# Kernel optimization log

Hardware: AMD Instinct MI355X
Metric: run time of the kernel (lower is better)

## Reference

```python
import jax, jax.numpy as jnp
import numpy as np

N = 50000   # nodes
E = 800000  # edges
G = 64      # graphs in the batch
DIN = 128
DOUT = 256


def _lin(key, fan_in, fan_out):
    s = 1.0 / np.sqrt(fan_in)
    kw, kb = jax.random.split(key)
    W = jax.random.uniform(kw, (fan_in, fan_out), jnp.float32, -s, s)
    b = jax.random.uniform(kb, (fan_out,), jnp.float32, -s, s)
    return W, b


def setup_inputs() -> dict:
    key = jax.random.key(0)
    ks = jax.random.split(key, 12)
    x = jax.random.normal(ks[0], (N, DIN), jnp.float32)
    edge_index = jax.random.randint(ks[1], (2, E), 0, N, dtype=jnp.int64)
    batch = jnp.sort(jax.random.randint(ks[2], (N,), 0, G, dtype=jnp.int64))
    W1, b1 = _lin(ks[3], DIN, 128)
    W2, b2 = _lin(ks[4], 128, 128)
    W3, b3 = _lin(ks[5], 128, 128)
    A1, ba1 = _lin(ks[6], DIN, 64)
    A2, ba2 = _lin(ks[7], 64, 32)
    A3, ba3 = _lin(ks[8], 32, 1)
    M1, bm1 = _lin(ks[9], 128, 128)
    M2, bm2 = _lin(ks[10], 128, DOUT)
    return dict(x=x, edge_index=edge_index, batch=batch,
                W1=W1, b1=b1, W2=W2, b2=b2, W3=W3, b3=b3,
                A1=A1, ba1=ba1, A2=A2, ba2=ba2, A3=A3, ba3=ba3,
                M1=M1, bm1=bm1, M2=M2, bm2=bm2)


def _gcn_norm(edge_index, n, dtype):
    # GCNConv default: add self-loops, symmetric normalization D^-1/2 (A+I) D^-1/2
    loop = jnp.arange(n, dtype=edge_index.dtype)
    src = jnp.concatenate([edge_index[0], loop])
    dst = jnp.concatenate([edge_index[1], loop])
    deg = jax.ops.segment_sum(jnp.ones_like(dst, dtype), dst, num_segments=n)
    dinv = jnp.where(deg > 0, jax.lax.rsqrt(deg), 0.0)
    return src, dst, dinv[src] * dinv[dst]


def _gcn(h, W, b, src, dst, norm, n):
    h = h @ W                                   # [N, F_out]
    msg = h[src] * norm[:, None]                # gather + scale (memory bound)
    return jax.ops.segment_sum(msg, dst, num_segments=n) + b


def _segment_softmax(w, batch, g):
    # per-graph softmax (PyG softmax): stabilize with segment max
    m = jax.ops.segment_max(w, batch, num_segments=g)
    e = jnp.exp(w - m[batch])
    s = jax.ops.segment_sum(e, batch, num_segments=g)
    return e / (s[batch] + 1e-16)


def reference(x, edge_index, batch,
              W1, b1, W2, b2, W3, b3,
              A1, ba1, A2, ba2, A3, ba3,
              M1, bm1, M2, bm2):
    n = x.shape[0]
    src, dst, norm = _gcn_norm(edge_index, n, x.dtype)
    relu = jax.nn.relu
    # feature branch
    f = relu(_gcn(x, W1, b1, src, dst, norm, n))
    f = relu(_gcn(f, W2, b2, src, dst, norm, n))
    f = relu(_gcn(f, W3, b3, src, dst, norm, n))
    # attention branch
    w = relu(_gcn(x, A1, ba1, src, dst, norm, n))
    w = relu(_gcn(w, A2, ba2, src, dst, norm, n))
    w = relu(_gcn(w, A3, ba3, src, dst, norm, n))   # [N, 1]
    w = _segment_softmax(w, batch, G)
    # attention-weighted sum pooling per graph
    pooled = jax.ops.segment_sum(f * w, batch, num_segments=G)  # [G, 128]
    # MLP([128,128,256], batch_norm=False): Linear+ReLU, plain last Linear
    out = relu(pooled @ M1 + bm1) @ M2 + bm2
    return out
```

## Files before the change

### kernel.cpp

```cpp
#include <hip/hip_runtime.h>
#include <hip/hip_fp16.h>
#include <math.h>


#define DIN 128
#define FH  128
#define DOUT 256
#define NBUK 128
#define SUBN 512
#define IMGCAP 16384
#define ECAP 16384

typedef float f4 __attribute__((ext_vector_type(4)));
typedef float f32x4 __attribute__((ext_vector_type(4)));
typedef _Float16 h8v __attribute__((ext_vector_type(8)));
typedef _Float16 h4v __attribute__((ext_vector_type(4)));


__global__ __launch_bounds__(256) void scan1_kernel(const int* __restrict__ cnt,
        int* __restrict__ bsum, float* __restrict__ dinv, int n) {
    __shared__ int sm[256];
    int tid = threadIdx.x;
    int base = blockIdx.x * 512;
    int a = (base + tid < n) ? cnt[base + tid] : 0;
    int b = (base + 256 + tid < n) ? cnt[base + 256 + tid] : 0;
    if (base + tid < n)       dinv[base + tid]       = rsqrtf((float)(a + 1));
    if (base + 256 + tid < n) dinv[base + 256 + tid] = rsqrtf((float)(b + 1));
    sm[tid] = a + b;
    __syncthreads();
    for (int off = 128; off > 0; off >>= 1) {
        if (tid < off) sm[tid] += sm[tid + off];
        __syncthreads();
    }
    if (tid == 0) bsum[blockIdx.x] = sm[0];
}

__global__ void scan2_kernel(const int* __restrict__ bsum, int* __restrict__ boff,
                             int* __restrict__ rpN, int nb) {
    if (threadIdx.x == 0) {
        int run = 0;
        for (int i = 0; i < nb; ++i) { boff[i] = run; run += bsum[i]; }
        *rpN = run;
    }
}

__global__ __launch_bounds__(256) void scan3_kernel(const int* __restrict__ cnt,
        const int* __restrict__ boff, int* __restrict__ rp, int n) {
    __shared__ int sm[256];
    int tid = threadIdx.x;
    int base = blockIdx.x * 512;
    int i0 = base + 2 * tid;
    int c0 = (i0 < n) ? cnt[i0] : 0;
    int c1 = (i0 + 1 < n) ? cnt[i0 + 1] : 0;
    int ps = c0 + c1;
    sm[tid] = ps;
    __syncthreads();
    for (int off = 1; off < 256; off <<= 1) {
        int v = (tid >= off) ? sm[tid - off] : 0;
        __syncthreads();
        sm[tid] += v;
        __syncthreads();
    }
    int excl = sm[tid] - ps + boff[blockIdx.x];
    if (i0 < n) rp[i0] = excl;
    if (i0 + 1 < n) rp[i0 + 1] = excl + c0;
}

__global__ __launch_bounds__(256) void ebucket_kernel(const int* __restrict__ src,
        const int* __restrict__ dst, int* __restrict__ bcur,
        unsigned long long* __restrict__ entries, int E, int shift) {
    __shared__ int lcnt[NBUK], lscan[NBUK], lbase[NBUK], lcur[NBUK];
    __shared__ unsigned long long stage[2048];
    const int tid = threadIdx.x;
    const int e0 = blockIdx.x * 2048;
    if (tid < NBUK) { lcnt[tid] = 0; lcur[tid] = 0; }
    __syncthreads();
    int s_[8], d_[8];
    #pragma unroll
    for (int k = 0; k < 8; ++k) {
        int e = e0 + k * 256 + tid;
        if (e < E) {
            s_[k] = src[e];
            d_[k] = dst[e];
            atomicAdd(&lcnt[d_[k] >> shift], 1);
        } else {
            d_[k] = -1;
        }
    }
    __syncthreads();
    if (tid < NBUK) lscan[tid] = lcnt[tid];
    __syncthreads();
    for (int off = 1; off < NBUK; off <<= 1) {
        int v = 0;
        if (tid < NBUK && tid >= off) v = lscan[tid - off];
        __syncthreads();
        if (tid < NBUK) lscan[tid] += v;
        __syncthreads();
    }
    if (tid < NBUK) {
        lscan[tid] -= lcnt[tid];
        lbase[tid] = lcnt[tid] ? atomicAdd(&bcur[tid], lcnt[tid]) : 0;
    }
    __syncthreads();
    #pragma unroll
    for (int k = 0; k < 8; ++k) {
        if (d_[k] >= 0) {
            int b = d_[k] >> shift;
            int pos = lscan[b] + atomicAdd(&lcur[b], 1);
            stage[pos] = ((unsigned long long)(unsigned)d_[k] << 32) | (unsigned)s_[k];
        }
    }
    __syncthreads();
    const int total = min(2048, E - e0);
    for (int i = tid; i < total; i += 256) {
        int lo = 0, hi = NBUK - 1;
        while (lo < hi) {
            int mid = (lo + hi + 1) >> 1;
            if (lscan[mid] <= i) lo = mid; else hi = mid - 1;
        }
        int idx = lbase[lo] + (i - lscan[lo]);
        if (idx < (lo + 1) * ECAP)
            entries[(size_t)idx] = stage[i];
    }
}

__global__ __launch_bounds__(512) void ecount_kernel(
        const unsigned long long* __restrict__ entries,
        const int* __restrict__ bcur, int* __restrict__ cnt, int n, int shift) {
    __shared__ int hist[SUBN];
    const int b = blockIdx.x;
    const int n0 = b << shift;
    if (n0 >= n) return;
    const int n1 = min(n0 + SUBN, n);
    const int tid = threadIdx.x;
    hist[tid] = 0;
    __syncthreads();
    const size_t ebase = (size_t)b * ECAP;
    const int len = min(bcur[b] - b * ECAP, ECAP);
    for (int i = tid; i < len; i += 512)
        atomicAdd(&hist[(int)(entries[ebase + i] >> 32) - n0], 1);
    __syncthreads();
    if (n0 + tid < n1) cnt[n0 + tid] = hist[tid];
}

__global__ __launch_bounds__(512) void ecsr_kernel(
        const unsigned long long* __restrict__ entries,
        const int* __restrict__ rp, const float* __restrict__ dinv,
        long long* __restrict__ cn, int n, int shift) {
    __shared__ long long img[IMGCAP];
    __shared__ int hist[SUBN];
    __shared__ int lcur[SUBN];
    __shared__ int sm[SUBN];
    __shared__ float dl[SUBN];
    const int b = blockIdx.x;
    const int n0 = b << shift;
    if (n0 >= n) return;
    const int n1 = min(n0 + (1 << shift), n);
    const int base = rp[n0];
    const int len  = rp[n1] - base;
    const size_t ebase = (size_t)b * ECAP;
    const int tid = threadIdx.x;
    hist[tid] = 0;
    lcur[tid] = 0;
    if (n0 + tid < n1) dl[tid] = dinv[n0 + tid];
    __syncthreads();
    for (int i = tid; i < len; i += 512)
        atomicAdd(&hist[(int)(entries[ebase + i] >> 32) - n0], 1);
    __syncthreads();
    int v = hist[tid];
    sm[tid] = v;
    __syncthreads();
    for (int off = 1; off < SUBN; off <<= 1) {
        int t = (tid >= off) ? sm[tid - off] : 0;
        __syncthreads();
        sm[tid] += t;
        __syncthreads();
    }
    hist[tid] = sm[tid] - v;
    __syncthreads();
    const bool fits = (len <= IMGCAP);
    for (int i = tid; i < len; i += 512) {
        unsigned long long e = entries[ebase + i];
        int d  = (int)(e >> 32) - n0;
        int sx = (int)(unsigned)(e & 0xffffffffu);
        int pos = hist[d] + atomicAdd(&lcur[d], 1);
        float w = dinv[sx] * dl[d];
        long long val = (long long)(unsigned)sx | ((long long)__float_as_int(w) << 32);
        if (fits) img[pos] = val;
        else      cn[base + pos] = val;
    }
    __syncthreads();
    if (fits)
        for (int i = tid; i < len; i += 512) cn[base + i] = img[i];
}

__global__ void gstart_kernel(const int* __restrict__ batch, int* __restrict__ gstart,
                              int n, int g) {
    int t = threadIdx.x;
    if (t > g) return;
    int lo = 0, hi = n;
    while (lo < hi) {
        int mid = (lo + hi) >> 1;
        if (batch[mid] < t) lo = mid + 1; else hi = mid;
    }
    gstart[t] = lo;
}

__global__ void cvt16_kernel(const float* __restrict__ in, __half* __restrict__ outh,
                             long n8) {
    long i = (long)blockIdx.x * 256 + threadIdx.x;
    if (i >= n8) return;
    f4 a = ((const f4*)in)[2 * i];
    f4 b = ((const f4*)in)[2 * i + 1];
    __half2 h0 = __float22half2_rn(make_float2(a.x, a.y));
    __half2 h1 = __float22half2_rn(make_float2(a.z, a.w));
    __half2 h2 = __float22half2_rn(make_float2(b.x, b.y));
    __half2 h3 = __float22half2_rn(make_float2(b.z, b.w));
    uint4 st;
    st.x = *(unsigned*)&h0; st.y = *(unsigned*)&h1;
    st.z = *(unsigned*)&h2; st.w = *(unsigned*)&h3;
    ((uint4*)outh)[i] = st;
}


__device__ __forceinline__ void wsplit(const float* __restrict__ W,
        _Float16* __restrict__ Th, _Float16* __restrict__ Tl,
        int fin, int fout, int i) {
    int r = i / fout, c = i % fout;
    float w = W[i];
    _Float16 h = (_Float16)w;
    Th[c * fin + r] = h;
    Tl[c * fin + r] = (_Float16)(w - (float)h);
}

__global__ __launch_bounds__(256) void wprep_kernel(const float* __restrict__ W1,
        const float* __restrict__ W2, const float* __restrict__ W3,
        const float* __restrict__ A1, const float* __restrict__ A2,
        _Float16* __restrict__ T, int* __restrict__ bcur) {
    int i = blockIdx.x * 256 + threadIdx.x;
    if (blockIdx.x == 0 && threadIdx.x < NBUK) bcur[threadIdx.x] = threadIdx.x * ECAP;
    if (i < 16384)       wsplit(W1, T,          T + 16384,  128, 128, i);
    else if (i < 32768)  wsplit(W2, T + 32768,  T + 49152,  128, 128, i - 16384);
    else if (i < 49152)  wsplit(W3, T + 65536,  T + 81920,  128, 128, i - 32768);
    else if (i < 57344)  wsplit(A1, T + 98304,  T + 106496, 128, 64,  i - 49152);
    else if (i < 59392)  wsplit(A2, T + 114688, T + 116736, 64,  32,  i - 57344);
}


__global__ __launch_bounds__(256) void fusedl1_kernel(const float* __restrict__ Y,
        const _Float16* __restrict__ T, const float* __restrict__ b1,
        const float* __restrict__ ba1, __half* __restrict__ t2,
        __half* __restrict__ u2, int n) {
    constexpr int LSTR  = 136;
    constexpr int LSTRB = 72;
    __shared__ _Float16 Yh[64 * LSTR], Yl[64 * LSTR];
    __shared__ _Float16 Fh[64 * LSTR], Fl[64 * LSTR];
    const int tid  = threadIdx.x;
    const int w    = tid >> 6;
    const int lane = tid & 63;
    const int bk   = (lane >> 4) * 8;
    const int cl   = lane & 15;
    const long row0 = (long)blockIdx.x * 64;

    for (int i = tid; i < 64 * 32; i += 256) {
        int r = i >> 5, c4 = i & 31;
        long gr = row0 + r;
        float4 v = {0.f, 0.f, 0.f, 0.f};
        if (gr < n) v = *(const float4*)&Y[gr * 128 + c4 * 4];
        _Float16 h0 = (_Float16)v.x, h1 = (_Float16)v.y;
        _Float16 h2 = (_Float16)v.z, h3 = (_Float16)v.w;
        *(h4v*)&Yh[r * LSTR + c4 * 4] = (h4v){h0, h1, h2, h3};
        *(h4v*)&Yl[r * LSTR + c4 * 4] =
            (h4v){(_Float16)(v.x - (float)h0), (_Float16)(v.y - (float)h1),
                  (_Float16)(v.z - (float)h2), (_Float16)(v.w - (float)h3)};
    }
    __syncthreads();

    {
        const _Float16* W1h = T;
        const _Float16* W1l = T + 16384;
        h8v Bh[2][4], Bl[2][4];
        #pragma unroll
        for (int ct = 0; ct < 2; ++ct) {
            int c = w * 32 + ct * 16 + cl;
            #pragma unroll
            for (int kk = 0; kk < 4; ++kk) {
                Bh[ct][kk] = *(const h8v*)&W1h[c * 128 + kk * 32 + bk];
                Bl[ct][kk] = *(const h8v*)&W1l[c * 128 + kk * 32 + bk];
            }
        }
        f32x4 acc[4][2];
        #pragma unroll
        for (int rt = 0; rt < 4; ++rt)
            #pragma unroll
            for (int ct = 0; ct < 2; ++ct) acc[rt][ct] = (f32x4){0.f,0.f,0.f,0.f};
        #pragma unroll
        for (int rt = 0; rt < 4; ++rt) {
            int r = rt * 16 + cl;
            #pragma unroll
            for (int kk = 0; kk < 4; ++kk) {
                h8v ah = *(const h8v*)&Yh[r * LSTR + kk * 32 + bk];
                h8v al = *(const h8v*)&Yl[r * LSTR + kk * 32 + bk];
                #pragma unroll
                for (int ct = 0; ct < 2; ++ct) {
                    acc[rt][ct] = __builtin_amdgcn_mfma_f32_16x16x32_f16(ah, Bh[ct][kk], acc[rt][ct], 0, 0, 0);
                    acc[rt][ct] = __builtin_amdgcn_mfma_f32_16x16x32_f16(ah, Bl[ct][kk], acc[rt][ct], 0, 0, 0);
                    acc[rt][ct] = __builtin_amdgcn_mfma_f32_16x16x32_f16(al, Bh[ct][kk], acc[rt][ct], 0, 0, 0);
                }
            }
        }
        #pragma unroll
        for (int rt = 0; rt < 4; ++rt) {
            int rowb = rt * 16 + (lane >> 4) * 4;
            #pragma unroll
            for (int ct = 0; ct < 2; ++ct) {
                int col = w * 32 + ct * 16 + cl;
                float bv = b1[col];
                #pragma unroll
                for (int j = 0; j < 4; ++j) {
                    float v = fmaxf(acc[rt][ct][j] + bv, 0.f);
                    _Float16 h = (_Float16)v;
                    Fh[(rowb + j) * LSTR + col] = h;
                    Fl[(rowb + j) * LSTR + col] = (_Float16)(v - (float)h);
                }
            }
        }
    }
    __syncthreads();

    {
        const _Float16* W2h = T + 32768;
        const _Float16* W2l = T + 49152;
        h8v Bh[2][4], Bl[2][4];
        #pragma unroll
        for (int ct = 0; ct < 2; ++ct) {
            int c = w * 32 + ct * 16 + cl;
            #pragma unroll
            for (int kk = 0; kk < 4; ++kk) {
                Bh[ct][kk] = *(const h8v*)&W2h[c * 128 + kk * 32 + bk];
                Bl[ct][kk] = *(const h8v*)&W2l[c * 128 + kk * 32 + bk];
            }
        }
        f32x4 acc[4][2];
        #pragma unroll
        for (int rt = 0; rt < 4; ++rt)
            #pragma unroll
            for (int ct = 0; ct < 2; ++ct) acc[rt][ct] = (f32x4){0.f,0.f,0.f,0.f};
        #pragma unroll
        for (int rt = 0; rt < 4; ++rt) {
            int r = rt * 16 + cl;
            #pragma unroll
            for (int kk = 0; kk < 4; ++kk) {
                h8v ah = *(const h8v*)&Fh[r * LSTR + kk * 32 + bk];
                h8v al = *(const h8v*)&Fl[r * LSTR + kk * 32 + bk];
                #pragma unroll
                for (int ct = 0; ct < 2; ++ct) {
                    acc[rt][ct] = __builtin_amdgcn_mfma_f32_16x16x32_f16(ah, Bh[ct][kk], acc[rt][ct], 0, 0, 0);
                    acc[rt][ct] = __builtin_amdgcn_mfma_f32_16x16x32_f16(ah, Bl[ct][kk], acc[rt][ct], 0, 0, 0);
                    acc[rt][ct] = __builtin_amdgcn_mfma_f32_16x16x32_f16(al, Bh[ct][kk], acc[rt][ct], 0, 0, 0);
                }
            }
        }
        __syncthreads();
        #pragma unroll
        for (int rt = 0; rt < 4; ++rt) {
            long rbase = row0 + rt * 16 + (lane >> 4) * 4;
            #pragma unroll
            for (int ct = 0; ct < 2; ++ct) {
                int col = w * 32 + ct * 16 + cl;
                #pragma unroll
                for (int j = 0; j < 4; ++j) {
                    long r = rbase + j;
                    if (r < n) t2[r * 128 + col] = __float2half(acc[rt][ct][j]);
                }
            }
        }
    }

    {
        const _Float16* A1h = T + 98304;
        const _Float16* A1l = T + 106496;
        int c = w * 16 + cl;
        h8v Bh[4], Bl[4];
        #pragma unroll
        for (int kk = 0; kk < 4; ++kk) {
            Bh[kk] = *(const h8v*)&A1h[c * 128 + kk * 32 + bk];
            Bl[kk] = *(const h8v*)&A1l[c * 128 + kk * 32 + bk];
        }
        f32x4 acc[4];
        #pragma unroll
        for (int rt = 0; rt < 4; ++rt) acc[rt] = (f32x4){0.f,0.f,0.f,0.f};
        #pragma unroll
        for (int rt = 0; rt < 4; ++rt) {
            int r = rt * 16 + cl;
            #pragma unroll
            for (int kk = 0; kk < 4; ++kk) {
                h8v ah = *(const h8v*)&Yh[r * LSTR + kk * 32 + bk];
                h8v al = *(const h8v*)&Yl[r * LSTR + kk * 32 + bk];
                acc[rt] = __builtin_amdgcn_mfma_f32_16x16x32_f16(ah, Bh[kk], acc[rt], 0, 0, 0);
                acc[rt] = __builtin_amdgcn_mfma_f32_16x16x32_f16(ah, Bl[kk], acc[rt], 0, 0, 0);
                acc[rt] = __builtin_amdgcn_mfma_f32_16x16x32_f16(al, Bh[kk], acc[rt], 0, 0, 0);
            }
        }
        float bv = ba1[c];
        #pragma unroll
        for (int rt = 0; rt < 4; ++rt) {
            int rowb = rt * 16 + (lane >> 4) * 4;
            #pragma unroll
            for (int j = 0; j < 4; ++j) {
                float v = fmaxf(acc[rt][j] + bv, 0.f);
                _Float16 h = (_Float16)v;
                Fh[(rowb + j) * LSTRB + c] = h;
                Fl[(rowb + j) * LSTRB + c] = (_Float16)(v - (float)h);
            }
        }
    }
    __syncthreads();

    if (w < 2) {
        const _Float16* A2h = T + 114688;
        const _Float16* A2l = T + 116736;
        int c = w * 16 + cl;
        h8v Bh[2], Bl[2];
        #pragma unroll
        for (int kk = 0; kk < 2; ++kk) {
            Bh[kk] = *(const h8v*)&A2h[c * 64 + kk * 32 + bk];
            Bl[kk] = *(const h8v*)&A2l[c * 64 + kk * 32 + bk];
        }
        f32x4 acc[4];
        #pragma unroll
        for (int rt = 0; rt < 4; ++rt) acc[rt] = (f32x4){0.f,0.f,0.f,0.f};
        #pragma unroll
        for (int rt = 0; rt < 4; ++rt) {
            int r = rt * 16 + cl;
            #pragma unroll
            for (int kk = 0; kk < 2; ++kk) {
                h8v ah = *(const h8v*)&Fh[r * LSTRB + kk * 32 + bk];
                h8v al = *(const h8v*)&Fl[r * LSTRB + kk * 32 + bk];
                acc[rt] = __builtin_amdgcn_mfma_f32_16x16x32_f16(ah, Bh[kk], acc[rt], 0, 0, 0);
                acc[rt] = __builtin_amdgcn_mfma_f32_16x16x32_f16(ah, Bl[kk], acc[rt], 0, 0, 0);
                acc[rt] = __builtin_amdgcn_mfma_f32_16x16x32_f16(al, Bh[kk], acc[rt], 0, 0, 0);
            }
        }
        #pragma unroll
        for (int rt = 0; rt < 4; ++rt) {
            long rbase = row0 + rt * 16 + (lane >> 4) * 4;
            #pragma unroll
            for (int j = 0; j < 4; ++j) {
                long r = rbase + j;
                if (r < n) u2[r * 32 + c] = __float2half(acc[rt][j]);
            }
        }
    }
}

template<int FIN, int FOUT, int OMODE>
__global__ __launch_bounds__(256) void mgemm_kernel(const float* __restrict__ A,
        const _Float16* __restrict__ Wh, const _Float16* __restrict__ Wl,
        const float* __restrict__ bias, void* __restrict__ Cv, int n) {
    constexpr int NWC  = (FOUT / 16 < 4) ? FOUT / 16 : 4;
    constexpr int NWR  = 4 / NWC;
    constexpr int BM   = 64 * NWR;
    constexpr int CT   = FOUT / 16 / NWC;
    constexpr int KS   = FIN / 32;
    constexpr int LSTR = FIN + 8;
    __shared__ _Float16 Ahs[BM * LSTR];
    __shared__ _Float16 Als[BM * LSTR];

    const int tid  = threadIdx.x;
    const int w    = tid >> 6;
    const int lane = tid & 63;
    const long row0 = (long)blockIdx.x * BM;

    for (int i = tid; i < BM * (FIN / 4); i += 256) {
        int r  = i / (FIN / 4);
        int c4 = i % (FIN / 4);
        long gr = row0 + r;
        float4 v = {0.f, 0.f, 0.f, 0.f};
        if (gr < n) v = *(const float4*)&A[gr * FIN + c4 * 4];
        _Float16 h0 = (_Float16)v.x, h1 = (_Float16)v.y;
        _Float16 h2 = (_Float16)v.z, h3 = (_Float16)v.w;
        h4v hh = {h0, h1, h2, h3};
        h4v ll = {(_Float16)(v.x - (float)h0), (_Float16)(v.y - (float)h1),
                  (_Float16)(v.z - (float)h2), (_Float16)(v.w - (float)h3)};
        *(h4v*)&Ahs[r * LSTR + c4 * 4] = hh;
        *(h4v*)&Als[r * LSTR + c4 * 4] = ll;
    }

    const int wc = w % NWC;
    const int wr = w / NWC;
    const int colbase = wc * CT * 16;
    const int bk = (lane >> 4) * 8;
    h8v Bh[CT][KS], Bl[CT][KS];
    #pragma unroll
    for (int ct = 0; ct < CT; ++ct) {
        int c = colbase + ct * 16 + (lane & 15);
        #pragma unroll
        for (int kk = 0; kk < KS; ++kk) {
            Bh[ct][kk] = *(const h8v*)&Wh[(size_t)c * FIN + kk * 32 + bk];
            Bl[ct][kk] = *(const h8v*)&Wl[(size_t)c * FIN + kk * 32 + bk];
        }
    }

    __syncthreads();

    f32x4 acc[4][CT];
    #pragma unroll
    for (int rt = 0; rt < 4; ++rt)
        #pragma unroll
        for (int ct = 0; ct < CT; ++ct)
            acc[rt][ct] = (f32x4){0.f, 0.f, 0.f, 0.f};

    #pragma unroll
    for (int rt = 0; rt < 4; ++rt) {
        const int r = wr * 64 + rt * 16 + (lane & 15);
        #pragma unroll
        for (int kk = 0; kk < KS; ++kk) {
            h8v ah = *(const h8v*)&Ahs[r * LSTR + kk * 32 + bk];
            h8v al = *(const h8v*)&Als[r * LSTR + kk * 32 + bk];
            #pragma unroll
            for (int ct = 0; ct < CT; ++ct) {
                acc[rt][ct] = __builtin_amdgcn_mfma_f32_16x16x32_f16(ah, Bh[ct][kk], acc[rt][ct], 0, 0, 0);
                acc[rt][ct] = __builtin_amdgcn_mfma_f32_16x16x32_f16(ah, Bl[ct][kk], acc[rt][ct], 0, 0, 0);
                acc[rt][ct] = __builtin_amdgcn_mfma_f32_16x16x32_f16(al, Bh[ct][kk], acc[rt][ct], 0, 0, 0);
            }
        }
    }

    #pragma unroll
    for (int rt = 0; rt < 4; ++rt) {
        const long rbase = row0 + wr * 64 + rt * 16 + (lane >> 4) * 4;
        #pragma unroll
        for (int ct = 0; ct < CT; ++ct) {
            const int col = colbase + ct * 16 + (lane & 15);
            if (OMODE == 1) {
                const float bv = bias[col];
                #pragma unroll
                for (int j = 0; j < 4; ++j) {
                    long r = rbase + j;
                    if (r < n)
                        ((float*)Cv)[r * FOUT + col] = fmaxf(acc[rt][ct][j] + bv, 0.f);
                }
            } else {
                #pragma unroll
                for (int j = 0; j < 4; ++j) {
                    long r = rbase + j;
                    if (r < n)
                        ((__half*)Cv)[r * FOUT + col] = __float2half(acc[rt][ct][j]);
                }
            }
        }
    }
}


__device__ __forceinline__ void hacc8(float acc[8], uint4 u, float w) {
    __half2 h; float2 f;
    h = *(__half2*)&u.x; f = __half22float2(h); acc[0] += w * f.x; acc[1] += w * f.y;
    h = *(__half2*)&u.y; f = __half22float2(h); acc[2] += w * f.x; acc[3] += w * f.y;
    h = *(__half2*)&u.z; f = __half22float2(h); acc[4] += w * f.x; acc[5] += w * f.y;
    h = *(__half2*)&u.w; f = __half22float2(h); acc[6] += w * f.x; acc[7] += w * f.y;
}

template<int F, bool BR>
__global__ __launch_bounds__(256) void aggh_kernel(const __half* __restrict__ tin,
        const float* __restrict__ bias, const float* __restrict__ dinv,
        const int* __restrict__ rp, const long long* __restrict__ cn,
        float* __restrict__ out, int n) {
    constexpr int LPR   = F / 8;
    constexpr int SLOTS = 64 / LPR;
    const int lane = threadIdx.x & 63;
    const int node = blockIdx.x * 4 + (threadIdx.x >> 6);
    if (node >= n) return;
    const int l    = lane % LPR;
    const int slot = lane / LPR;
    const uint4* base = (const uint4*)tin + l;
    const int e0 = rp[node], e1 = rp[node + 1];
    float acc[8] = {0.f, 0.f, 0.f, 0.f, 0.f, 0.f, 0.f, 0.f};
    if (slot == 0) {
        float di = dinv[node];
        uint4 u = base[(size_t)node * LPR];
        hacc8(acc, u, di * di);
    }
    int p = e0 + slot;
    for (; p + 3 * SLOTS < e1; p += 4 * SLOTS) {
        long long r0 = __builtin_nontemporal_load(cn + p);
        long long r1 = __builtin_nontemporal_load(cn + p + SLOTS);
        long long r2 = __builtin_nontemporal_load(cn + p + 2 * SLOTS);
        long long r3 = __builtin_nontemporal_load(cn + p + 3 * SLOTS);
        uint4 u0 = base[(size_t)(unsigned)r0 * LPR];
        uint4 u1 = base[(size_t)(unsigned)r1 * LPR];
        uint4 u2 = base[(size_t)(unsigned)r2 * LPR];
        uint4 u3 = base[(size_t)(unsigned)r3 * LPR];
        hacc8(acc, u0, __int_as_float((int)(r0 >> 32)));
        hacc8(acc, u1, __int_as_float((int)(r1 >> 32)));
        hacc8(acc, u2, __int_as_float((int)(r2 >> 32)));
        hacc8(acc, u3, __int_as_float((int)(r3 >> 32)));
    }
    for (; p + SLOTS < e1; p += 2 * SLOTS) {
        long long r0 = __builtin_nontemporal_load(cn + p);
        long long r1 = __builtin_nontemporal_load(cn + p + SLOTS);
        uint4 u0 = base[(size_t)(unsigned)r0 * LPR];
        uint4 u1 = base[(size_t)(unsigned)r1 * LPR];
        hacc8(acc, u0, __int_as_float((int)(r0 >> 32)));
        hacc8(acc, u1, __int_as_float((int)(r1 >> 32)));
    }
    if (p < e1) {
        long long r0 = __builtin_nontemporal_load(cn + p);
        uint4 u0 = base[(size_t)(unsigned)r0 * LPR];
        hacc8(acc, u0, __int_as_float((int)(r0 >> 32)));
    }
    #pragma unroll
    for (int off = 32; off >= LPR; off >>= 1) {
        #pragma unroll
        for (int j = 0; j < 8; ++j) acc[j] += __shfl_xor(acc[j], off);
    }
    if (slot == 0) {
        if (BR) {
            #pragma unroll
            for (int j = 0; j < 8; ++j)
                acc[j] = fmaxf(acc[j] + bias[l * 8 + j], 0.f);
        }
        f4 lo = {acc[0], acc[1], acc[2], acc[3]};
        f4 hi = {acc[4], acc[5], acc[6], acc[7]};
        float* o = out + (size_t)node * F + l * 8;
        __builtin_nontemporal_store(lo, (f4*)o);
        __builtin_nontemporal_store(hi, (f4*)(o + 4));
    }
}

__global__ __launch_bounds__(256) void aggh32a_kernel(const __half* __restrict__ tin,
        const float* __restrict__ ba2, const float* __restrict__ A3,
        const float* __restrict__ dinv, const int* __restrict__ rp,
        const long long* __restrict__ cn, float* __restrict__ wlin, int n) {
    constexpr int LPR   = 4;
    constexpr int SLOTS = 16;
    const int lane = threadIdx.x & 63;
    const int node = blockIdx.x * 4 + (threadIdx.x >> 6);
    if (node >= n) return;
    const int l    = lane % LPR;
    const int slot = lane / LPR;
    const uint4* base = (const uint4*)tin + l;
    const int e0 = rp[node], e1 = rp[node + 1];
    float acc[8] = {0.f, 0.f, 0.f, 0.f, 0.f, 0.f, 0.f, 0.f};
    if (slot == 0) {
        float di = dinv[node];
        uint4 u = base[(size_t)node * LPR];
        hacc8(acc, u, di * di);
    }
    int p = e0 + slot;
    for (; p + SLOTS < e1; p += 2 * SLOTS) {
        long long r0 = __builtin_nontemporal_load(cn + p);
        long long r1 = __builtin_nontemporal_load(cn + p + SLOTS);
        uint4 u0 = base[(size_t)(unsigned)r0 * LPR];
        uint4 u1 = base[(size_t)(unsigned)r1 * LPR];
        hacc8(acc, u0, __int_as_float((int)(r0 >> 32)));
        hacc8(acc, u1, __int_as_float((int)(r1 >> 32)));
    }
    if (p < e1) {
        long long r0 = __builtin_nontemporal_load(cn + p);
        uint4 u0 = base[(size_t)(unsigned)r0 * LPR];
        hacc8(acc, u0, __int_as_float((int)(r0 >> 32)));
    }
    #pragma unroll
    for (int off = 32; off >= LPR; off >>= 1) {
        #pragma unroll
        for (int j = 0; j < 8; ++j) acc[j] += __shfl_xor(acc[j], off);
    }
    if (slot == 0) {
        float part = 0.f;
        #pragma unroll
        for (int j = 0; j < 8; ++j)
            part += fmaxf(acc[j] + ba2[l * 8 + j], 0.f) * A3[l * 8 + j];
        part += __shfl_xor(part, 1);
        part += __shfl_xor(part, 2);
        if (l == 0) wlin[node] = part;
    }
}

__global__ void agg1_kernel(const float* __restrict__ tin, const float* __restrict__ bias,
        const float* __restrict__ dinv, const int* __restrict__ rp,
        const long long* __restrict__ cn, float* __restrict__ out, int n) {
    int i = blockIdx.x * 256 + threadIdx.x;
    if (i >= n) return;
    float di = dinv[i];
    float acc = di * di * tin[i];
    int e0 = rp[i], e1 = rp[i + 1];
    int p = e0;
    float a0 = 0.f, a1 = 0.f, a2 = 0.f, a3 = 0.f;
    for (; p + 3 < e1; p += 4) {
        long long r0 = __builtin_nontemporal_load(cn + p);
        long long r1 = __builtin_nontemporal_load(cn + p + 1);
        long long r2 = __builtin_nontemporal_load(cn + p + 2);
        long long r3 = __builtin_nontemporal_load(cn + p + 3);
        a0 += __int_as_float((int)(r0 >> 32)) * tin[(int)(unsigned)r0];
        a1 += __int_as_float((int)(r1 >> 32)) * tin[(int)(unsigned)r1];
        a2 += __int_as_float((int)(r2 >> 32)) * tin[(int)(unsigned)r2];
        a3 += __int_as_float((int)(r3 >> 32)) * tin[(int)(unsigned)r3];
    }
    for (; p < e1; ++p) {
        long long r0 = __builtin_nontemporal_load(cn + p);
        a0 += __int_as_float((int)(r0 >> 32)) * tin[(int)(unsigned)r0];
    }
    acc += a0 + a1 + a2 + a3 + bias[0];
    out[i] = acc > 0.f ? acc : 0.f;
}


__global__ __launch_bounds__(256) void smexp_kernel(const float* __restrict__ w,
        const int* __restrict__ gstart, float* __restrict__ gsum,
        float* __restrict__ e) {
    const int g = blockIdx.x;
    const int a = gstart[g], b = gstart[g + 1];
    const int tid = threadIdx.x;
    __shared__ float red[4];
    float m = 0.f;
    for (int i = a + tid; i < b; i += 256) m = fmaxf(m, w[i]);
    #pragma unroll
    for (int off = 32; off > 0; off >>= 1) m = fmaxf(m, __shfl_xor(m, off));
    if ((tid & 63) == 0) red[tid >> 6] = m;
    __syncthreads();
    m = fmaxf(fmaxf(red[0], red[1]), fmaxf(red[2], red[3]));
    float s = 0.f;
    for (int i = a + tid; i < b; i += 256) {
        float ex = expf(w[i] - m);
        e[i] = ex;
        s += ex;
    }
    #pragma unroll
    for (int off = 32; off > 0; off >>= 1) s += __shfl_xor(s, off);
    __syncthreads();
    if ((tid & 63) == 0) red[tid >> 6] = s;
    __syncthreads();
    if (tid == 0) gsum[g] = red[0] + red[1] + red[2] + red[3];
}


__global__ __launch_bounds__(128) void pool_kernel(const float* __restrict__ f3,
        const float* __restrict__ e, const float* __restrict__ gsum,
        const int* __restrict__ gstart, float* __restrict__ pooled) {
    constexpr int SPG = 64;
    const int g = blockIdx.x / SPG, s = blockIdx.x % SPG;
    const int a = gstart[g], bnd = gstart[g + 1];
    const int len = bnd - a;
    if (len <= 0) return;
    const int chunk = (len + SPG - 1) / SPG;
    const int lo = a + s * chunk;
    const int hi = min(lo + chunk, bnd);
    if (lo >= hi) return;
    const float inv = 1.f / (gsum[g] + 1e-16f);
    const int tid = threadIdx.x;
    const int lane4 = tid & 31;
    const int rs    = tid >> 5;
    f4 acc = {0.f, 0.f, 0.f, 0.f};
    for (int i = lo + rs; i < hi; i += 4) {
        float w = e[i] * inv;
        f4 v = *(const f4*)&f3[(size_t)i * FH + lane4 * 4];
        acc.x += w * v.x; acc.y += w * v.y;
        acc.z += w * v.z; acc.w += w * v.w;
    }
    acc.x += __shfl_xor(acc.x, 32);
    acc.y += __shfl_xor(acc.y, 32);
    acc.z += __shfl_xor(acc.z, 32);
    acc.w += __shfl_xor(acc.w, 32);
    __shared__ float sm[128];
    if (tid >= 64 && tid < 96) *(f4*)&sm[(tid - 64) * 4] = acc;
    __syncthreads();
    if (tid < 32) {
        f4 o = *(f4*)&sm[tid * 4];
        o.x += acc.x; o.y += acc.y; o.z += acc.z; o.w += acc.w;
        float* dst = &pooled[g * FH + tid * 4];
        atomicAdd(dst + 0, o.x);
        atomicAdd(dst + 1, o.y);
        atomicAdd(dst + 2, o.z);
        atomicAdd(dst + 3, o.w);
    }
}


__global__ __launch_bounds__(128) void mlp1_kernel(const float* __restrict__ pooled,
        const float* __restrict__ M1, const float* __restrict__ bm1,
        float* __restrict__ hidden) {
    __shared__ float pr[FH];
    int g = blockIdx.x, j = threadIdx.x;
    pr[j] = pooled[g * FH + j];
    __syncthreads();
    float acc = bm1[j];
    #pragma unroll 8
    for (int k = 0; k < FH; ++k) acc += pr[k] * M1[k * FH + j];
    hidden[g * FH + j] = acc > 0.f ? acc : 0.f;
}

__global__ __launch_bounds__(256) void mlp2_kernel(const float* __restrict__ hidden,
        const float* __restrict__ M2, const float* __restrict__ bm2,
        float* __restrict__ out) {
    __shared__ float hr[FH];
    int g = blockIdx.x, j = threadIdx.x;
    if (j < FH) hr[j] = hidden[g * FH + j];
    __syncthreads();
    float acc = bm2[j];
    #pragma unroll 8
    for (int k = 0; k < FH; ++k) acc += hr[k] * M2[k * DOUT + j];
    out[g * DOUT + j] = acc;
}


extern "C" void kernel_launch(void* const* d_in, const int* in_sizes, int n_in,
                              void* d_out, int out_size, void* d_ws, size_t ws_size,
                              hipStream_t stream) {
    const float* x   = (const float*)d_in[0];
    const int*   ei  = (const int*)d_in[1];
    const int*   batch = (const int*)d_in[2];
    const float* W1  = (const float*)d_in[3];
    const float* b1  = (const float*)d_in[4];
    const float* W2  = (const float*)d_in[5];
    const float* b2  = (const float*)d_in[6];
    const float* W3  = (const float*)d_in[7];
    const float* b3  = (const float*)d_in[8];
    const float* A1  = (const float*)d_in[9];
    const float* ba1 = (const float*)d_in[10];
    const float* A2  = (const float*)d_in[11];
    const float* ba2 = (const float*)d_in[12];
    const float* A3  = (const float*)d_in[13];
    const float* ba3 = (const float*)d_in[14];
    const float* M1  = (const float*)d_in[15];
    const float* bm1 = (const float*)d_in[16];
    const float* M2  = (const float*)d_in[17];
    const float* bm2 = (const float*)d_in[18];

    const int N = in_sizes[0] / DIN;
    const int E = in_sizes[1] / 2;
    const int G = out_size / DOUT;
    const int* src = ei;
    const int* dst = ei + E;
    float* out = (float*)d_out;

    int shift = 9;
    while (((N + (1 << shift) - 1) >> shift) > NBUK) ++shift;
    const int nbuckets = (N + (1 << shift) - 1) >> shift;

    char* p = (char*)d_ws;
    auto alloc = [&](size_t bytes) -> void* {
        void* r = (void*)p;
        p += (bytes + 255) & ~(size_t)255;
        return r;
    };
    float* dinv  = (float*)alloc((size_t)N * 4);
    int*   cnt   = (int*)alloc((size_t)N * 4);
    int*   rp    = (int*)alloc((size_t)(N + 1) * 4);
    long long* cn = (long long*)alloc((size_t)E * 8);
    float* SY    = (float*)alloc((size_t)N * FH * 4);
    float* SA    = (float*)alloc((size_t)N * FH * 4);
    __half* ST   = (__half*)alloc((size_t)N * FH * 2);
    char*  SX    = (char*)alloc((size_t)N * 256);
    __half* u2   = (__half*)alloc((size_t)N * 32 * 2);
    float* wlin  = (float*)alloc((size_t)N * 4);
    float* wact  = (float*)alloc((size_t)N * 4);
    float* ebuf  = (float*)alloc((size_t)N * 4);
    float* gsum  = (float*)alloc((size_t)G * 4);
    int*   gstart= (int*)alloc((size_t)(G + 1) * 4);
    float* pooled= (float*)alloc((size_t)G * FH * 4);
    float* hidden= (float*)alloc((size_t)G * FH * 4);
    int*   bsum  = (int*)alloc(256 * 4);
    int*   boff  = (int*)alloc(256 * 4);
    int*   bcur  = (int*)alloc(NBUK * 4);
    _Float16* WT = (_Float16*)alloc((size_t)118784 * 2);

    __half* xh = (__half*)SX;
    unsigned long long* entries = (unsigned long long*)SA;

    hipMemsetAsync(pooled, 0, (size_t)G * FH * 4, stream);

    const int nb = (N + 255) / 256;
    const int NB = (N + 511) / 512;

    wprep_kernel<<<232, 256, 0, stream>>>(W1, W2, W3, A1, A2, WT, bcur);
    ebucket_kernel<<<(E + 2047) / 2048, 256, 0, stream>>>(src, dst, bcur, entries, E, shift);
    ecount_kernel<<<nbuckets, 512, 0, stream>>>(entries, bcur, cnt, N, shift);
    scan1_kernel<<<NB, 256, 0, stream>>>(cnt, bsum, dinv, N);
    scan2_kernel<<<1, 64, 0, stream>>>(bsum, boff, rp + N, NB);
    scan3_kernel<<<NB, 256, 0, stream>>>(cnt, boff, rp, N);
    gstart_kernel<<<1, 128, 0, stream>>>(batch, gstart, N, G);
    ecsr_kernel<<<nbuckets, 512, 0, stream>>>(entries, rp, dinv, cn, N, shift);

    const long n8 = (long)N * FH / 8;
    cvt16_kernel<<<(int)((n8 + 255) / 256), 256, 0, stream>>>(x, xh, n8);

    const int gb64 = (N + 63) / 64;
    const int agb  = (N + 3) / 4;

    aggh_kernel<FH, false><<<agb, 256, 0, stream>>>(xh, nullptr, dinv, rp, cn, SY, N);

    fusedl1_kernel<<<gb64, 256, 0, stream>>>(SY, WT, b1, ba1, (__half*)ST, u2, N);

    aggh_kernel<FH, true><<<agb, 256, 0, stream>>>(ST, b2, dinv, rp, cn, SA, N);
    mgemm_kernel<FH, FH, 2><<<gb64, 256, 0, stream>>>(SA, WT + 65536, WT + 81920, nullptr, ST, N);
    aggh_kernel<FH, true><<<agb, 256, 0, stream>>>(ST, b3, dinv, rp, cn, SY, N);

    aggh32a_kernel<<<agb, 256, 0, stream>>>(u2, ba2, A3, dinv, rp, cn, wlin, N);
    agg1_kernel<<<nb, 256, 0, stream>>>(wlin, ba3, dinv, rp, cn, wact, N);

    smexp_kernel<<<G, 256, 0, stream>>>(wact, gstart, gsum, ebuf);
    pool_kernel<<<G * 64, 128, 0, stream>>>(SY, ebuf, gsum, gstart, pooled);

    mlp1_kernel<<<G, 128, 0, stream>>>(pooled, M1, bm1, hidden);
    mlp2_kernel<<<G, 256, 0, stream>>>(hidden, M2, bm2, out);
}
```

Measured before the change: 309.9 us.

## Restructure fused layer-1 kernel to cut LDS and rebalance attention GEMM

```diff
diff --git a/kernel.cpp b/kernel.cpp
--- a/kernel.cpp
+++ b/kernel.cpp
@@ -247,20 +247,35 @@
 }
 
 
-__global__ __launch_bounds__(256) void fusedl1_kernel(const float* __restrict__ Y,
+__global__ __launch_bounds__(256, 3) void fusedl1_kernel(const float* __restrict__ Y,
         const _Float16* __restrict__ T, const float* __restrict__ b1,
         const float* __restrict__ ba1, __half* __restrict__ t2,
         __half* __restrict__ u2, int n) {
     constexpr int LSTR  = 136;
-    constexpr int LSTRB = 72;
-    __shared__ _Float16 Yh[64 * LSTR], Yl[64 * LSTR];
-    __shared__ _Float16 Fh[64 * LSTR], Fl[64 * LSTR];
+    constexpr int LSTRB = 68;
+    __shared__ _Float16 L1[64 * LSTR];
+    __shared__ _Float16 L2[64 * LSTR];
+    __shared__ _Float16 Ah_[64 * LSTRB];
+    __shared__ _Float16 Al_[64 * LSTRB];
     const int tid  = threadIdx.x;
     const int w    = tid >> 6;
     const int lane = tid & 63;
     const int bk   = (lane >> 4) * 8;
     const int cl   = lane & 15;
     const long row0 = (long)blockIdx.x * 64;
+
+    const _Float16* W1h = T;
+    const _Float16* W1l = T + 16384;
+    h8v W1hf[2][4], W1lf[2][4];
+    #pragma unroll
+    for (int ct = 0; ct < 2; ++ct) {
+        int c = w * 32 + ct * 16 + cl;
+        #pragma unroll
+        for (int kk = 0; kk < 4; ++kk) {
+            W1hf[ct][kk] = *(const h8v*)&W1h[c * 128 + kk * 32 + bk];
+            W1lf[ct][kk] = *(const h8v*)&W1l[c * 128 + kk * 32 + bk];
+        }
+    }
 
     for (int i = tid; i < 64 * 32; i += 256) {
         int r = i >> 5, c4 = i & 31;
@@ -269,24 +284,103 @@
         if (gr < n) v = *(const float4*)&Y[gr * 128 + c4 * 4];
         _Float16 h0 = (_Float16)v.x, h1 = (_Float16)v.y;
         _Float16 h2 = (_Float16)v.z, h3 = (_Float16)v.w;
-        *(h4v*)&Yh[r * LSTR + c4 * 4] = (h4v){h0, h1, h2, h3};
-        *(h4v*)&Yl[r * LSTR + c4 * 4] =
+        *(h4v*)&L1[r * LSTR + c4 * 4] = (h4v){h0, h1, h2, h3};
+        *(h4v*)&L2[r * LSTR + c4 * 4] =
             (h4v){(_Float16)(v.x - (float)h0), (_Float16)(v.y - (float)h1),
                   (_Float16)(v.z - (float)h2), (_Float16)(v.w - (float)h3)};
     }
     __syncthreads();
 
+    f32x4 accF[4][2];
+    #pragma unroll
+    for (int rt = 0; rt < 4; ++rt)
+        #pragma unroll
+        for (int ct = 0; ct < 2; ++ct) accF[rt][ct] = (f32x4){0.f,0.f,0.f,0.f};
+    #pragma unroll
+    for (int rt = 0; rt < 4; ++rt) {
+        int r = rt * 16 + cl;
+        #pragma unroll
+        for (int kk = 0; kk < 4; ++kk) {
+            h8v ah = *(const h8v*)&L1[r * LSTR + kk * 32 + bk];
+            h8v al = *(const h8v*)&L2[r * LSTR + kk * 32 + bk];
+            #pragma unroll
+            for (int ct = 0; ct < 2; ++ct) {
+                accF[rt][ct] = __builtin_amdgcn_mfma_f32_16x16x32_f16(ah, W1hf[ct][kk], accF[rt][ct], 0, 0, 0);
+                accF[rt][ct] = __builtin_amdgcn_mfma_f32_16x16x32_f16(ah, W1lf[ct][kk], accF[rt][ct], 0, 0, 0);
+                accF[rt][ct] = __builtin_amdgcn_mfma_f32_16x16x32_f16(al, W1hf[ct][kk], accF[rt][ct], 0, 0, 0);
+            }
+        }
+    }
+
+    const _Float16* A1h = T + 98304;
+    const _Float16* A1l = T + 106496;
+    const int ca = w * 16 + cl;
+    h8v A1hf[4], A1lf[4];
+    #pragma unroll
+    for (int kk = 0; kk < 4; ++kk) {
+        A1hf[kk] = *(const h8v*)&A1h[ca * 128 + kk * 32 + bk];
+        A1lf[kk] = *(const h8v*)&A1l[ca * 128 + kk * 32 + bk];
+    }
+    f32x4 accA[4];
+    #pragma unroll
+    for (int rt = 0; rt < 4; ++rt) accA[rt] = (f32x4){0.f,0.f,0.f,0.f};
+    #pragma unroll
+    for (int rt = 0; rt < 4; ++rt) {
+        int r = rt * 16 + cl;
+        #pragma unroll
+        for (int kk = 0; kk < 4; ++kk) {
+            h8v ah = *(const h8v*)&L1[r * LSTR + kk * 32 + bk];
+            h8v al = *(const h8v*)&L2[r * LSTR + kk * 32 + bk];
+            accA[rt] = __builtin_amdgcn_mfma_f32_16x16x32_f16(ah, A1hf[kk], accA[rt], 0, 0, 0);
+            accA[rt] = __builtin_amdgcn_mfma_f32_16x16x32_f16(ah, A1lf[kk], accA[rt], 0, 0, 0);
+            accA[rt] = __builtin_amdgcn_mfma_f32_16x16x32_f16(al, A1hf[kk], accA[rt], 0, 0, 0);
+        }
+    }
+    __syncthreads();
+
+    #pragma unroll
+    for (int rt = 0; rt < 4; ++rt) {
+        int rowb = rt * 16 + (lane >> 4) * 4;
+        #pragma unroll
+        for (int ct = 0; ct < 2; ++ct) {
+            int col = w * 32 + ct * 16 + cl;
+            float bv = b1[col];
+            #pragma unroll
+            for (int j = 0; j < 4; ++j) {
+                float v = fmaxf(accF[rt][ct][j] + bv, 0.f);
+                _Float16 h = (_Float16)v;
+                L1[(rowb + j) * LSTR + col] = h;
+                L2[(rowb + j) * LSTR + col] = (_Float16)(v - (float)h);
+            }
+        }
+    }
     {
-        const _Float16* W1h = T;
-        const _Float16* W1l = T + 16384;
+        float bv = ba1[ca];
+        #pragma unroll
+        for (int rt = 0; rt < 4; ++rt) {
+            int rowb = rt * 16 + (lane >> 4) * 4;
+            #pragma unroll
+            for (int j = 0; j < 4; ++j) {
+                float v = fmaxf(accA[rt][j] + bv, 0.f);
+                _Float16 h = (_Float16)v;
+                Ah_[(rowb + j) * LSTRB + ca] = h;
+                Al_[(rowb + j) * LSTRB + ca] = (_Float16)(v - (float)h);
+            }
+        }
+    }
+    __syncthreads();
+
+    {
+        const _Float16* W2h = T + 32768;
+        const _Float16* W2l = T + 49152;
         h8v Bh[2][4], Bl[2][4];
         #pragma unroll
         for (int ct = 0; ct < 2; ++ct) {
             int c = w * 32 + ct * 16 + cl;
             #pragma unroll
             for (int kk = 0; kk < 4; ++kk) {
-                Bh[ct][kk] = *(const h8v*)&W1h[c * 128 + kk * 32 + bk];
-                Bl[ct][kk] = *(const h8v*)&W1l[c * 128 + kk * 32 + bk];
+                Bh[ct][kk] = *(const h8v*)&W2h[c * 128 + kk * 32 + bk];
+                Bl[ct][kk] = *(const h8v*)&W2l[c * 128 + kk * 32 + bk];
             }
         }
         f32x4 acc[4][2];
@@ -299,8 +393,8 @@
             int r = rt * 16 + cl;
             #pragma unroll
             for (int kk = 0; kk < 4; ++kk) {
-                h8v ah = *(const h8v*)&Yh[r * LSTR + kk * 32 + bk];
-                h8v al = *(const h8v*)&Yl[r * LSTR + kk * 32 + bk];
+                h8v ah = *(const h8v*)&L1[r * LSTR + kk * 32 + bk];
+                h8v al = *(const h8v*)&L2[r * LSTR + kk * 32 + bk];
                 #pragma unroll
                 for (int ct = 0; ct < 2; ++ct) {
                     acc[rt][ct] = __builtin_amdgcn_mfma_f32_16x16x32_f16(ah, Bh[ct][kk], acc[rt][ct], 0, 0, 0);
@@ -309,59 +403,6 @@
                 }
             }
         }
-        #pragma unroll
-        for (int rt = 0; rt < 4; ++rt) {
-            int rowb = rt * 16 + (lane >> 4) * 4;
-            #pragma unroll
-            for (int ct = 0; ct < 2; ++ct) {
-                int col = w * 32 + ct * 16 + cl;
-                float bv = b1[col];
-                #pragma unroll
-                for (int j = 0; j < 4; ++j) {
-                    float v = fmaxf(acc[rt][ct][j] + bv, 0.f);
-                    _Float16 h = (_Float16)v;
-                    Fh[(rowb + j) * LSTR + col] = h;
-                    Fl[(rowb + j) * LSTR + col] = (_Float16)(v - (float)h);
-                }
-            }
-        }
-    }
-    __syncthreads();
-
-    {
-        const _Float16* W2h = T + 32768;
-        const _Float16* W2l = T + 49152;
-        h8v Bh[2][4], Bl[2][4];
-        #pragma unroll
-        for (int ct = 0; ct < 2; ++ct) {
-            int c = w * 32 + ct * 16 + cl;
-            #pragma unroll
-            for (int kk = 0; kk < 4; ++kk) {
-                Bh[ct][kk] = *(const h8v*)&W2h[c * 128 + kk * 32 + bk];
-                Bl[ct][kk] = *(const h8v*)&W2l[c * 128 + kk * 32 + bk];
-            }
-        }
-        f32x4 acc[4][2];
-        #pragma unroll
-        for (int rt = 0; rt < 4; ++rt)
-            #pragma unroll
-            for (int ct = 0; ct < 2; ++ct) acc[rt][ct] = (f32x4){0.f,0.f,0.f,0.f};
-        #pragma unroll
-        for (int rt = 0; rt < 4; ++rt) {
-            int r = rt * 16 + cl;
-            #pragma unroll
-            for (int kk = 0; kk < 4; ++kk) {
-                h8v ah = *(const h8v*)&Fh[r * LSTR + kk * 32 + bk];
-                h8v al = *(const h8v*)&Fl[r * LSTR + kk * 32 + bk];
-                #pragma unroll
-                for (int ct = 0; ct < 2; ++ct) {
-                    acc[rt][ct] = __builtin_amdgcn_mfma_f32_16x16x32_f16(ah, Bh[ct][kk], acc[rt][ct], 0, 0, 0);
-                    acc[rt][ct] = __builtin_amdgcn_mfma_f32_16x16x32_f16(ah, Bl[ct][kk], acc[rt][ct], 0, 0, 0);
-                    acc[rt][ct] = __builtin_amdgcn_mfma_f32_16x16x32_f16(al, Bh[ct][kk], acc[rt][ct], 0, 0, 0);
-                }
-            }
-        }
-        __syncthreads();
         #pragma unroll
         for (int rt = 0; rt < 4; ++rt) {
             long rbase = row0 + rt * 16 + (lane >> 4) * 4;
@@ -378,77 +419,41 @@
     }
 
     {
-        const _Float16* A1h = T + 98304;
-        const _Float16* A1l = T + 106496;
-        int c = w * 16 + cl;
-        h8v Bh[4], Bl[4];
-        #pragma unroll
-        for (int kk = 0; kk < 4; ++kk) {
-            Bh[kk] = *(const h8v*)&A1h[c * 128 + kk * 32 + bk];
-            Bl[kk] = *(const h8v*)&A1l[c * 128 + kk * 32 + bk];
-        }
-        f32x4 acc[4];
-        #pragma unroll
-        for (int rt = 0; rt < 4; ++rt) acc[rt] = (f32x4){0.f,0.f,0.f,0.f};
-        #pragma unroll
-        for (int rt = 0; rt < 4; ++rt) {
-            int r = rt * 16 + cl;
-            #pragma unroll
-            for (int kk = 0; kk < 4; ++kk) {
-                h8v ah = *(const h8v*)&Yh[r * LSTR + kk * 32 + bk];
-                h8v al = *(const h8v*)&Yl[r * LSTR + kk * 32 + bk];
-                acc[rt] = __builtin_amdgcn_mfma_f32_16x16x32_f16(ah, Bh[kk], acc[rt], 0, 0, 0);
-                acc[rt] = __builtin_amdgcn_mfma_f32_16x16x32_f16(ah, Bl[kk], acc[rt], 0, 0, 0);
-                acc[rt] = __builtin_amdgcn_mfma_f32_16x16x32_f16(al, Bh[kk], acc[rt], 0, 0, 0);
-            }
-        }
-        float bv = ba1[c];
-        #pragma unroll
-        for (int rt = 0; rt < 4; ++rt) {
-            int rowb = rt * 16 + (lane >> 4) * 4;
-            #pragma unroll
-            for (int j = 0; j < 4; ++j) {
-                float v = fmaxf(acc[rt][j] + bv, 0.f);
-                _Float16 h = (_Float16)v;
-                Fh[(rowb + j) * LSTRB + c] = h;
-                Fl[(rowb + j) * LSTRB + c] = (_Float16)(v - (float)h);
-            }
-        }
-    }
-    __syncthreads();
-
-    if (w < 2) {
         const _Float16* A2h = T + 114688;
         const _Float16* A2l = T + 116736;
-        int c = w * 16 + cl;
-        h8v Bh[2], Bl[2];
+        h8v Bh[2][2], Bl[2][2];
+        #pragma unroll
+        for (int ct = 0; ct < 2; ++ct) {
+            int c = ct * 16 + cl;
+            #pragma unroll
+            for (int kk = 0; kk < 2; ++kk) {
+                Bh[ct][kk] = *(const h8v*)&A2h[c * 64 + kk * 32 + bk];
+                Bl[ct][kk] = *(const h8v*)&A2l[c * 64 + kk * 32 + bk];
+            }
+        }
+        f32x4 acc[2];
+        acc[0] = (f32x4){0.f,0.f,0.f,0.f};
+        acc[1] = (f32x4){0.f,0.f,0.f,0.f};
+        const int r = w * 16 + cl;
         #pragma unroll
         for (int kk = 0; kk < 2; ++kk) {
-            Bh[kk] = *(const h8v*)&A2h[c * 64 + kk * 32 + bk];
-            Bl[kk] = *(const h8v*)&A2l[c * 64 + kk * 32 + bk];
-        }
-        f32x4 acc[4];
-        #pragma unroll
-        for (int rt = 0; rt < 4; ++rt) acc[rt] = (f32x4){0.f,0.f,0.f,0.f};
-        #pragma unroll
-        for (int rt = 0; rt < 4; ++rt) {
-            int r = rt * 16 + cl;
-            #pragma unroll
-            for (int kk = 0; kk < 2; ++kk) {
-                h8v ah = *(const h8v*)&Fh[r * LSTRB + kk * 32 + bk];
-                h8v al = *(const h8v*)&Fl[r * LSTRB + kk * 32 + bk];
-                acc[rt] = __builtin_amdgcn_mfma_f32_16x16x32_f16(ah, Bh[kk], acc[rt], 0, 0, 0);
-                acc[rt] = __builtin_amdgcn_mfma_f32_16x16x32_f16(ah, Bl[kk], acc[rt], 0, 0, 0);
-                acc[rt] = __builtin_amdgcn_mfma_f32_16x16x32_f16(al, Bh[kk], acc[rt], 0, 0, 0);
-            }
-        }
-        #pragma unroll
-        for (int rt = 0; rt < 4; ++rt) {
-            long rbase = row0 + rt * 16 + (lane >> 4) * 4;
+            h8v ah = *(const h8v*)&Ah_[r * LSTRB + kk * 32 + bk];
+            h8v al = *(const h8v*)&Al_[r * LSTRB + kk * 32 + bk];
+            #pragma unroll
+            for (int ct = 0; ct < 2; ++ct) {
+                acc[ct] = __builtin_amdgcn_mfma_f32_16x16x32_f16(ah, Bh[ct][kk], acc[ct], 0, 0, 0);
+                acc[ct] = __builtin_amdgcn_mfma_f32_16x16x32_f16(ah, Bl[ct][kk], acc[ct], 0, 0, 0);
+                acc[ct] = __builtin_amdgcn_mfma_f32_16x16x32_f16(al, Bh[ct][kk], acc[ct], 0, 0, 0);
+            }
+        }
+        long rbase = row0 + w * 16 + (lane >> 4) * 4;
+        #pragma unroll
+        for (int ct = 0; ct < 2; ++ct) {
+            int col = ct * 16 + cl;
             #pragma unroll
             for (int j = 0; j < 4; ++j) {
-                long r = rbase + j;
-                if (r < n) u2[r * 32 + c] = __float2half(acc[rt][j]);
+                long rr = rbase + j;
+                if (rr < n) u2[rr * 32 + col] = __float2half(acc[ct][j]);
             }
         }
     }
```

Measured after the change: 316.6 us. 2.2% more time.
